# Kernel tuning notes

Hardware: AMD Instinct MI355X
Metric: run time of the kernel (lower is better)

## Reference

```python
import jax, jax.numpy as jnp
import numpy as np

B, T, F, U = 32768, 7, 36, 256

def setup_inputs() -> dict:
    key = jax.random.key(0)
    ks = jax.random.split(key, 5)
    x = jax.random.normal(ks[0], (B, T, F), dtype=jnp.float32)
    h0 = jax.random.normal(ks[1], (B, U), dtype=jnp.float32)
    c0 = jax.random.normal(ks[2], (B, U), dtype=jnp.float32)
    Wk = jax.random.normal(ks[3], (F, 4 * U), dtype=jnp.float32) * 0.1
    Wr = jax.random.normal(ks[4], (U, 4 * U), dtype=jnp.float32) * 0.05
    b = jnp.zeros((4 * U,), dtype=jnp.float32)
    return {"x": x, "h0": h0, "c0": c0, "Wk": Wk, "Wr": Wr, "b": b}

def reference(x, h0, c0, Wk, Wr, b):
    # Precompute input projection for all 7 steps: [B,T,4U]
    zx = jnp.einsum('btf,fg->btg', x, Wk) + b
    zx_t = jnp.transpose(zx, (1, 0, 2))  # time-major [T,B,4U]

    def step(carry, z_in):
        h, c = carry
        z = z_in + h @ Wr  # [B,4U]
        i, f, g, o = jnp.split(z, 4, axis=-1)  # Keras gate order i,f,g,o
        i = jax.nn.sigmoid(i)
        f = jax.nn.sigmoid(f)
        g = jnp.tanh(g)
        o = jax.nn.sigmoid(o)
        c_new = f * c + i * g
        h_new = o * jnp.tanh(c_new)
        return (h_new, c_new), h_new

    (_, _), hs = jax.lax.scan(step, (h0, c0), zx_t)
    return jnp.transpose(hs, (1, 0, 2))  # [B,T,U] (return_sequences=True)
```

## Files before the change

kernel.cpp:

```cpp
#include <hip/hip_runtime.h>
#include <hip/hip_bf16.h>

typedef _Float16 half8 __attribute__((ext_vector_type(8)));
typedef float f32x4 __attribute__((ext_vector_type(4)));

#define B_TOTAL 32768
#define T 7
#define F 36
#define U 256
#define G4 1024
#define BM 64
#define KC 10
#define KPACK 32
#define H_STRIDE 264
#define X_STRIDE 72

__global__ __launch_bounds__(1024) void pack_w(const float* __restrict__ Wr,
                                               const float* __restrict__ Wk,
                                               _Float16* __restrict__ Wq) {
    const int kc   = blockIdx.x >> 2;
    const int kin0 = (blockIdx.x & 3) * 8;
    const int n    = threadIdx.x;
    _Float16* dst = Wq + ((size_t)kc * G4 + n) * KPACK + kin0;
    #pragma unroll
    for (int j = 0; j < 8; ++j) {
        int k = kc * KPACK + kin0 + j;
        float v = 0.f;
        if (k < U)          v = Wr[(size_t)k * G4 + n];
        else if (k < U + F) v = Wk[(size_t)(k - U) * G4 + n];
        dst[j] = (_Float16)v;
    }
}

__device__ __forceinline__ float fast_sigmoid(float x) {
    return __builtin_amdgcn_rcpf(1.f + __expf(-x));
}
__device__ __forceinline__ float fast_tanh(float x) {
    return 1.f - 2.f * __builtin_amdgcn_rcpf(1.f + __expf(2.f * x));
}

__global__ __launch_bounds__(1024) void lstm_kernel(
    const float* __restrict__ x,
    const float* __restrict__ h0,
    const float* __restrict__ c0,
    const _Float16* __restrict__ Wq,
    const float* __restrict__ bias_g,
    float* __restrict__ out)
{
    __shared__ __align__(16) _Float16 hA[BM * H_STRIDE];
    __shared__ __align__(16) _Float16 xA[BM * X_STRIDE];

    const int tid  = threadIdx.x;
    const int lane = tid & 63;
    const int w    = tid >> 6;
    const int l15  = lane & 15;
    const int q    = lane >> 4;
    const int u0   = w * 16;
    const int b0   = blockIdx.x * BM;

    for (int i = tid; i < BM * U; i += 1024) {
        int m = i >> 8, u = i & 255;
        hA[m * H_STRIDE + u] = (_Float16)h0[(size_t)b0 * U + i];
    }
    for (int i = tid; i < BM * (64 - F); i += 1024) {
        int m = i / (64 - F), f = i % (64 - F);
        xA[m * X_STRIDE + F + f] = (_Float16)0.f;
    }
    for (int i = tid; i < BM * F; i += 1024) {
        int m = i / F, f = i % F;
        xA[m * X_STRIDE + f] = (_Float16)x[((size_t)(b0 + m) * T) * F + f];
    }
    float c[16];
    #pragma unroll
    for (int mt = 0; mt < 4; ++mt)
        #pragma unroll
        for (int r = 0; r < 4; ++r) {
            int row = mt * 16 + q * 4 + r;
            c[mt * 4 + r] = c0[(size_t)(b0 + row) * U + u0 + l15];
        }
    float bv[4];
    #pragma unroll
    for (int g = 0; g < 4; ++g) bv[g] = bias_g[g * U + u0 + l15];

    __syncthreads();

    for (int t = 0; t < T; ++t) {
        f32x4 acc[4][4];
        #pragma unroll
        for (int mt = 0; mt < 4; ++mt)
            #pragma unroll
            for (int g = 0; g < 4; ++g)
                acc[mt][g] = (f32x4){bv[g], bv[g], bv[g], bv[g]};

        float xp0 = 0.f, xp1 = 0.f, xp2 = 0.f;
        if (t + 1 < T) {
            {
                int i = tid;        int m = i / F, f = i % F;
                xp0 = x[((size_t)(b0 + m) * T + t + 1) * F + f];
            }
            {
                int i = tid + 1024; int m = i / F, f = i % F;
                xp1 = x[((size_t)(b0 + m) * T + t + 1) * F + f];
            }
            if (tid < BM * F - 2048) {
                int i = tid + 2048; int m = i / F, f = i % F;
                xp2 = x[((size_t)(b0 + m) * T + t + 1) * F + f];
            }
        }

        #pragma unroll 2
        for (int kc = 0; kc < KC; ++kc) {
            half8 bf[4];
            #pragma unroll
            for (int g = 0; g < 4; ++g) {
                size_t off = ((size_t)kc * G4 + g * U + u0 + l15) * KPACK + q * 8;
                bf[g] = *(const half8*)(Wq + off);
            }
            #pragma unroll
            for (int mt = 0; mt < 4; ++mt) {
                half8 af;
                if (kc < 8)
                    af = *(const half8*)&hA[(mt * 16 + l15) * H_STRIDE + kc * 32 + q * 8];
                else
                    af = *(const half8*)&xA[(mt * 16 + l15) * X_STRIDE + (kc - 8) * 32 + q * 8];
                #pragma unroll
                for (int g = 0; g < 4; ++g)
                    acc[mt][g] = __builtin_amdgcn_mfma_f32_16x16x32_f16(af, bf[g], acc[mt][g], 0, 0, 0);
            }
        }

        float hnew[16];
        #pragma unroll
        for (int mt = 0; mt < 4; ++mt)
            #pragma unroll
            for (int r = 0; r < 4; ++r) {
                float zi = acc[mt][0][r];
                float zf = acc[mt][1][r];
                float zg = acc[mt][2][r];
                float zo = acc[mt][3][r];
                float ig = fast_sigmoid(zi);
                float fg = fast_sigmoid(zf);
                float gg = fast_tanh(zg);
                float og = fast_sigmoid(zo);
                float cn = fg * c[mt * 4 + r] + ig * gg;
                c[mt * 4 + r] = cn;
                hnew[mt * 4 + r] = og * fast_tanh(cn);
            }

        __syncthreads();

        #pragma unroll
        for (int mt = 0; mt < 4; ++mt)
            #pragma unroll
            for (int r = 0; r < 4; ++r) {
                int row = mt * 16 + q * 4 + r;
                hA[row * H_STRIDE + u0 + l15] = (_Float16)hnew[mt * 4 + r];
            }
        if (t + 1 < T) {
            { int i = tid;        int m = i / F, f = i % F; xA[m * X_STRIDE + f] = (_Float16)xp0; }
            { int i = tid + 1024; int m = i / F, f = i % F; xA[m * X_STRIDE + f] = (_Float16)xp1; }
            if (tid < BM * F - 2048) {
                int i = tid + 2048; int m = i / F, f = i % F;
                xA[m * X_STRIDE + f] = (_Float16)xp2;
            }
        }
        __syncthreads();

        #pragma unroll
        for (int rb = 0; rb < 2; ++rb) {
            int j   = tid + rb * 1024;
            int row = j >> 5;
            int uo  = (j & 31) * 8;
            half8 hv = *(const half8*)&hA[row * H_STRIDE + uo];
            f32x4 lo = { (float)hv[0], (float)hv[1], (float)hv[2], (float)hv[3] };
            f32x4 hi = { (float)hv[4], (float)hv[5], (float)hv[6], (float)hv[7] };
            float* dst = out + ((size_t)(b0 + row) * T + t) * U + uo;
            *(f32x4*)dst       = lo;
            *(f32x4*)(dst + 4) = hi;
        }
    }
}

extern "C" void kernel_launch(void* const* d_in, const int* in_sizes, int n_in,
                              void* d_out, int out_size, void* d_ws, size_t ws_size,
                              hipStream_t stream) {
    const float* x  = (const float*)d_in[0];
    const float* h0 = (const float*)d_in[1];
    const float* c0 = (const float*)d_in[2];
    const float* Wk = (const float*)d_in[3];
    const float* Wr = (const float*)d_in[4];
    const float* b  = (const float*)d_in[5];
    float* out = (float*)d_out;

    _Float16* Wq = (_Float16*)d_ws;

    pack_w<<<KC * 4, 1024, 0, stream>>>(Wr, Wk, Wq);
    lstm_kernel<<<B_TOTAL / BM, 1024, 0, stream>>>(x, h0, c0, Wq, b, out);
}
```

Baseline: 514.6 us.

## Double-buffer hidden state and preload all timesteps of x into LDS

Stages the full x tile for all 7 timesteps into shared memory up front and double-buffers the fp16 hidden state. Each thread writes its new h directly into the alternate buffer, which removes one block barrier per step and the per-step x prefetch through registers. Shared memory use grows substantially, which can drop residency from two blocks to one per CU and reduce latency hiding.

```diff
diff --git a/kernel.cpp b/kernel.cpp
--- a/kernel.cpp
+++ b/kernel.cpp
@@ -1,5 +1,4 @@
 #include <hip/hip_runtime.h>
-#include <hip/hip_bf16.h>
 
 typedef _Float16 half8 __attribute__((ext_vector_type(8)));
 typedef float f32x4 __attribute__((ext_vector_type(4)));
@@ -13,7 +12,7 @@
 #define KC 10
 #define KPACK 32
 #define H_STRIDE 264
-#define X_STRIDE 72
+#define XS 72
 
 __global__ __launch_bounds__(1024) void pack_w(const float* __restrict__ Wr,
                                                const float* __restrict__ Wk,
@@ -47,8 +46,8 @@
     const float* __restrict__ bias_g,
     float* __restrict__ out)
 {
-    __shared__ __align__(16) _Float16 hA[BM * H_STRIDE];
-    __shared__ __align__(16) _Float16 xA[BM * X_STRIDE];
+    __shared__ __align__(16) _Float16 hbuf[2][BM * H_STRIDE];
+    __shared__ __align__(16) _Float16 xs[T * BM * XS];
 
     const int tid  = threadIdx.x;
     const int lane = tid & 63;
@@ -58,17 +57,23 @@
     const int u0   = w * 16;
     const int b0   = blockIdx.x * BM;
 
+    {
+        half8 z = {};
+        for (int i = tid * 8; i < T * BM * XS; i += 1024 * 8)
+            *(half8*)&xs[i] = z;
+    }
+    __syncthreads();
+
     for (int i = tid; i < BM * U; i += 1024) {
         int m = i >> 8, u = i & 255;
-        hA[m * H_STRIDE + u] = (_Float16)h0[(size_t)b0 * U + i];
+        hbuf[0][m * H_STRIDE + u] = (_Float16)h0[(size_t)b0 * U + i];
     }
-    for (int i = tid; i < BM * (64 - F); i += 1024) {
-        int m = i / (64 - F), f = i % (64 - F);
-        xA[m * X_STRIDE + F + f] = (_Float16)0.f;
-    }
-    for (int i = tid; i < BM * F; i += 1024) {
-        int m = i / F, f = i % F;
-        xA[m * X_STRIDE + f] = (_Float16)x[((size_t)(b0 + m) * T) * F + f];
+    for (int i = tid; i < BM * (T * F); i += 1024) {
+        int row = i / (T * F);
+        int rem = i - row * (T * F);
+        int t   = rem / F;
+        int f   = rem - t * F;
+        xs[(t * BM + row) * XS + f] = (_Float16)x[(size_t)(b0 + row) * (T * F) + rem];
     }
     float c[16];
     #pragma unroll
@@ -84,6 +89,8 @@
 
     __syncthreads();
 
+    int cur = 0;
+    #pragma unroll 1
     for (int t = 0; t < T; ++t) {
         f32x4 acc[4][4];
         #pragma unroll
@@ -91,22 +98,6 @@
             #pragma unroll
             for (int g = 0; g < 4; ++g)
                 acc[mt][g] = (f32x4){bv[g], bv[g], bv[g], bv[g]};
-
-        float xp0 = 0.f, xp1 = 0.f, xp2 = 0.f;
-        if (t + 1 < T) {
-            {
-                int i = tid;        int m = i / F, f = i % F;
-                xp0 = x[((size_t)(b0 + m) * T + t + 1) * F + f];
-            }
-            {
-                int i = tid + 1024; int m = i / F, f = i % F;
-                xp1 = x[((size_t)(b0 + m) * T + t + 1) * F + f];
-            }
-            if (tid < BM * F - 2048) {
-                int i = tid + 2048; int m = i / F, f = i % F;
-                xp2 = x[((size_t)(b0 + m) * T + t + 1) * F + f];
-            }
-        }
 
         #pragma unroll 2
         for (int kc = 0; kc < KC; ++kc) {
@@ -120,16 +111,16 @@
             for (int mt = 0; mt < 4; ++mt) {
                 half8 af;
                 if (kc < 8)
-                    af = *(const half8*)&hA[(mt * 16 + l15) * H_STRIDE + kc * 32 + q * 8];
+                    af = *(const half8*)&hbuf[cur][(mt * 16 + l15) * H_STRIDE + kc * 32 + q * 8];
                 else
-                    af = *(const half8*)&xA[(mt * 16 + l15) * X_STRIDE + (kc - 8) * 32 + q * 8];
+                    af = *(const half8*)&xs[(t * BM + mt * 16 + l15) * XS + (kc - 8) * 32 + q * 8];
                 #pragma unroll
                 for (int g = 0; g < 4; ++g)
                     acc[mt][g] = __builtin_amdgcn_mfma_f32_16x16x32_f16(af, bf[g], acc[mt][g], 0, 0, 0);
             }
         }
 
-        float hnew[16];
+        const int nxt = cur ^ 1;
         #pragma unroll
         for (int mt = 0; mt < 4; ++mt)
             #pragma unroll
@@ -144,26 +135,11 @@
                 float og = fast_sigmoid(zo);
                 float cn = fg * c[mt * 4 + r] + ig * gg;
                 c[mt * 4 + r] = cn;
-                hnew[mt * 4 + r] = og * fast_tanh(cn);
+                float hv = og * fast_tanh(cn);
+                int row = mt * 16 + q * 4 + r;
+                hbuf[nxt][row * H_STRIDE + u0 + l15] = (_Float16)hv;
             }
 
-        __syncthreads();
-
-        #pragma unroll
-        for (int mt = 0; mt < 4; ++mt)
-            #pragma unroll
-            for (int r = 0; r < 4; ++r) {
-                int row = mt * 16 + q * 4 + r;
-                hA[row * H_STRIDE + u0 + l15] = (_Float16)hnew[mt * 4 + r];
-            }
-        if (t + 1 < T) {
-            { int i = tid;        int m = i / F, f = i % F; xA[m * X_STRIDE + f] = (_Float16)xp0; }
-            { int i = tid + 1024; int m = i / F, f = i % F; xA[m * X_STRIDE + f] = (_Float16)xp1; }
-            if (tid < BM * F - 2048) {
-                int i = tid + 2048; int m = i / F, f = i % F;
-                xA[m * X_STRIDE + f] = (_Float16)xp2;
-            }
-        }
         __syncthreads();
 
         #pragma unroll
@@ -171,13 +147,15 @@
             int j   = tid + rb * 1024;
             int row = j >> 5;
             int uo  = (j & 31) * 8;
-            half8 hv = *(const half8*)&hA[row * H_STRIDE + uo];
+            half8 hv = *(const half8*)&hbuf[nxt][row * H_STRIDE + uo];
             f32x4 lo = { (float)hv[0], (float)hv[1], (float)hv[2], (float)hv[3] };
             f32x4 hi = { (float)hv[4], (float)hv[5], (float)hv[6], (float)hv[7] };
             float* dst = out + ((size_t)(b0 + row) * T + t) * U + uo;
             *(f32x4*)dst       = lo;
             *(f32x4*)(dst + 4) = hi;
         }
+
+        cur = nxt;
     }
 }
 
```

After: 486.2 us. 5.5% less time.
